# Kernel tuning notes

Hardware: AMD Instinct MI355X
Metric: run time of the kernel (lower is better)

The kernel has to match this reference:

```python
import jax, jax.numpy as jnp
import numpy as np

TOPK = 13
ALPHA = 1.0
BETA = 6.0
NUM_CLASSES = 80
EPS = 1e-9


def _make_boxes(key, shape, max_half):
    # shape = (..., 4): build valid x1y1x2y2 boxes inside a 640x640 image
    kc, ks = jax.random.split(key)
    centers = jax.random.uniform(kc, shape[:-1] + (2,), minval=30.0, maxval=610.0)
    halves = jax.random.uniform(ks, shape[:-1] + (2,), minval=2.0, maxval=max_half)
    return jnp.concatenate([centers - halves, centers + halves], axis=-1)


def setup_inputs() -> dict:
    key = jax.random.key(0)
    k1, k2, k3, k4, k5 = jax.random.split(key, 5)
    B, L, C, n = 16, 8400, NUM_CLASSES, 128
    pred_scores = jax.random.uniform(k1, (B, L, C), dtype=jnp.float32)
    pred_bboxes = _make_boxes(k2, (B, L, 4), 60.0)
    anchor_points = jax.random.uniform(k3, (L, 2), minval=0.0, maxval=640.0)
    gt_labels = jax.random.randint(k4, (B, n), 0, C, dtype=jnp.int32)
    gt_bboxes = _make_boxes(k5, (B, n, 4), 120.0)
    pad_gt_mask = jnp.ones((B, n, 1), dtype=jnp.float32)
    return {"pred_scores": pred_scores, "pred_bboxes": pred_bboxes,
            "anchor_points": anchor_points, "gt_labels": gt_labels,
            "gt_bboxes": gt_bboxes, "pad_gt_mask": pad_gt_mask}


def _batch_iou(box1, box2, eps=1e-9):
    # box1: [B, n, 4], box2: [B, L, 4] -> iou [B, n, L]
    b1 = box1[:, :, None]  # [B,n,1,4]
    b2 = box2[:, None]     # [B,1,L,4]
    x1y1 = jnp.maximum(b1[..., 0:2], b2[..., 0:2])
    x2y2 = jnp.minimum(b1[..., 2:4], b2[..., 2:4])
    overlap = jnp.prod(jnp.clip(x2y2 - x1y1, 0.0), axis=-1)
    area1 = jnp.prod(jnp.clip(b1[..., 2:4] - b1[..., 0:2], 0.0), axis=-1)
    area2 = jnp.prod(jnp.clip(b2[..., 2:4] - b2[..., 0:2], 0.0), axis=-1)
    return overlap / (area1 + area2 - overlap + eps)


def _points_in_bboxes(points, bboxes, eps=EPS):
    # points: [L,2], bboxes: [B,n,4] -> [B,n,L] float
    x = points[None, None, :, 0]
    y = points[None, None, :, 1]
    xmin = bboxes[..., 0:1]; ymin = bboxes[..., 1:2]
    xmax = bboxes[..., 2:3]; ymax = bboxes[..., 3:4]
    l = x - xmin; t = y - ymin; r = xmax - x; b = ymax - y
    d = jnp.minimum(jnp.minimum(l, t), jnp.minimum(r, b))
    return (d > eps).astype(bboxes.dtype)


def _gather_topk(metrics, topk, topk_mask):
    # metrics: [B,n,L] -> one-hot membership of per-gt topk anchors [B,n,L]
    L = metrics.shape[-1]
    _, topk_idxs = jax.lax.top_k(metrics, topk)          # [B,n,topk]
    is_in_topk = jax.nn.one_hot(topk_idxs, L, dtype=metrics.dtype).sum(-2)
    return is_in_topk * topk_mask


def reference(pred_scores, pred_bboxes, anchor_points, gt_labels, gt_bboxes, pad_gt_mask):
    B, n, _ = gt_bboxes.shape
    L = pred_bboxes.shape[1]
    # pairwise IoU between gts and predicted boxes: [B,n,L]
    ious = _batch_iou(gt_bboxes, pred_bboxes)
    # per-gt class scores gathered from pred_scores: [B,n,L]
    scores_cl = jnp.transpose(pred_scores, (0, 2, 1))                 # [B,C,L]
    bbox_cls_scores = jnp.take_along_axis(scores_cl, gt_labels[:, :, None].astype(jnp.int32), axis=1)
    # task-aligned metric
    alignment = (bbox_cls_scores ** ALPHA) * (ious ** BETA)
    is_in_gts = _points_in_bboxes(anchor_points, gt_bboxes)           # [B,n,L]
    is_in_topk = _gather_topk(alignment * is_in_gts, TOPK, pad_gt_mask)
    mask_positive = is_in_topk * is_in_gts * pad_gt_mask              # [B,n,L]
    # resolve anchors assigned to multiple gts: keep max-IoU gt
    mask_pos_sum = mask_positive.sum(-2)                              # [B,L]
    is_max_iou = jnp.transpose(jax.nn.one_hot(jnp.argmax(ious, axis=-2), n, dtype=ious.dtype), (0, 2, 1))
    mask_positive = jnp.where((mask_pos_sum[:, None, :] > 1), is_max_iou, mask_positive)
    mask_pos_sum = mask_positive.sum(-2)
    # assignment
    assigned_gt_index = jnp.argmax(mask_positive, axis=-2)            # [B,L]
    flat_idx = assigned_gt_index + jnp.arange(B, dtype=assigned_gt_index.dtype)[:, None] * n
    assigned_labels = jnp.reshape(gt_labels, (-1,))[flat_idx]
    assigned_labels = jnp.where(mask_pos_sum > 0, assigned_labels, NUM_CLASSES)
    assigned_bboxes = jnp.reshape(gt_bboxes, (-1, 4))[flat_idx]       # [B,L,4]
    assigned_scores = jax.nn.one_hot(assigned_labels, NUM_CLASSES + 1, dtype=pred_scores.dtype)[..., :NUM_CLASSES]
    # rescale scores by normalized alignment metric
    align_m = alignment * mask_positive
    max_metric = align_m.max(-1, keepdims=True)                       # [B,n,1]
    max_iou = (ious * mask_positive).max(-1, keepdims=True)           # [B,n,1]
    align_m = (align_m / (max_metric + EPS)) * max_iou
    assigned_scores = assigned_scores * align_m.max(-2)[..., None]    # [B,L,C]
    return assigned_labels, assigned_bboxes, assigned_scores
```

## Files before the change

### kernel.cpp

```cpp
#include <hip/hip_runtime.h>
#include <stdint.h>

#define BB    16
#define NGT   128
#define LL    8400
#define CC    80
#define KTOP  13
#define FEPS  1e-9f
#define NCELL 10
#define SLOTS 128

typedef float vfloat4 __attribute__((ext_vector_type(4)));

__device__ __forceinline__ float iou_f(float4 g, float4 p) {
    float ix0 = fmaxf(g.x, p.x);
    float iy0 = fmaxf(g.y, p.y);
    float ix1 = fminf(g.z, p.z);
    float iy1 = fminf(g.w, p.w);
    float ow = fmaxf(ix1 - ix0, 0.0f);
    float oh = fmaxf(iy1 - iy0, 0.0f);
    float ov = ow * oh;
    float a1 = fmaxf(g.z - g.x, 0.0f) * fmaxf(g.w - g.y, 0.0f);
    float a2 = fmaxf(p.z - p.x, 0.0f) * fmaxf(p.w - p.y, 0.0f);
    return ov / (a1 + a2 - ov + FEPS);
}

#define SORT2(a,b) { unsigned long long _t=(a), _u=(b); (a)=(_u>_t)?_u:_t; (b)=(_u>_t)?_t:_u; }
#define INSERT13(key) do { unsigned long long _k=(key); if (_k > k12) { k12=_k; \
    SORT2(k11,k12) SORT2(k10,k11) SORT2(k9,k10) SORT2(k8,k9) SORT2(k7,k8) \
    SORT2(k6,k7)  SORT2(k5,k6)  SORT2(k4,k5) SORT2(k3,k4) SORT2(k2,k3) \
    SORT2(k1,k2)  SORT2(k0,k1) } } while(0)
#define POP13() { k0=k1;k1=k2;k2=k3;k3=k4;k4=k5;k5=k6;k6=k7;k7=k8;k8=k9;k9=k10;k10=k11;k11=k12;k12=0ull; }

__global__ __launch_bounds__(256) void prep_kernel(
    const float2* __restrict__ anchors,
    int* __restrict__ bin_cnt,
    int* __restrict__ bins,
    int* __restrict__ zero_base,
    int  zero_words)
{
    int blk = blockIdx.x;
    int tid = threadIdx.x;
    if (blk < NCELL * NCELL) {
        __shared__ int lcnt;
        __shared__ int lbin[SLOTS];
        if (tid == 0) lcnt = 0;
        __syncthreads();
        int cy = blk / NCELL, cx = blk % NCELL;
        for (int j = tid; j < LL; j += 256) {
            float2 ap = anchors[j];
            int acx = min(max((int)(ap.x * (1.0f / 64.0f)), 0), NCELL - 1);
            int acy = min(max((int)(ap.y * (1.0f / 64.0f)), 0), NCELL - 1);
            if (acx == cx && acy == cy) {
                int s = atomicAdd(&lcnt, 1);
                if (s < SLOTS) lbin[s] = j;
            }
        }
        __syncthreads();
        if (tid == 0) bin_cnt[blk] = lcnt;
        int n = min(lcnt, SLOTS);
        for (int s = tid; s < n; s += 256) bins[blk * SLOTS + s] = lbin[s];
    } else {
        int t = (blk - NCELL * NCELL) * 256 + tid;
        if (t < zero_words) zero_base[t] = 0;
    }
}

__global__ __launch_bounds__(256) void select_kernel(
    const float*  __restrict__ pred_scores,
    const float4* __restrict__ pred_bboxes,
    const float2* __restrict__ anchors,
    const int*    __restrict__ gt_labels,
    const float4* __restrict__ gt_bboxes,
    const int*    __restrict__ bin_cnt,
    const int*    __restrict__ bins,
    int* __restrict__ claim_count,
    int* __restrict__ claimant)
{
    int tid  = threadIdx.x;
    int wave = tid >> 6;
    int lane = tid & 63;
    int row  = blockIdx.x;
    int b    = row >> 7;
    int i_gt = row & (NGT - 1);

    float4 g  = gt_bboxes[row];
    int label = gt_labels[row];
    const float*  sc = pred_scores + (size_t)b * LL * CC + label;
    const float4* pb = pred_bboxes + (size_t)b * LL;

    unsigned long long k0=0,k1=0,k2=0,k3=0,k4=0,k5=0,k6=0,k7=0,k8=0,k9=0,k10=0,k11=0,k12=0;

    int cx0 = min(max((int)(g.x * (1.0f / 64.0f)), 0), NCELL - 1);
    int cy0 = min(max((int)(g.y * (1.0f / 64.0f)), 0), NCELL - 1);
    int cx1 = min(max((int)(g.z * (1.0f / 64.0f)), 0), NCELL - 1);
    int cy1 = min(max((int)(g.w * (1.0f / 64.0f)), 0), NCELL - 1);
    int ncx = cx1 - cx0 + 1;
    int ncells = ncx * (cy1 - cy0 + 1);

    bool ovf = false;
    for (int c = 0; c < ncells; ++c) {
        int cell = (cy0 + c / ncx) * NCELL + (cx0 + c % ncx);
        if (bin_cnt[cell] > SLOTS) ovf = true;
    }

    if (ovf) {
        for (int j = tid; j < LL; j += 256) {
            float2 ap = anchors[j];
            float d = fminf(fminf(ap.x - g.x, ap.y - g.y),
                            fminf(g.z - ap.x, g.w - ap.y));
            if (d > FEPS) {
                float4 p = pb[j];
                float io = iou_f(g, p);
                if (io > 0.0f) {
                    float s  = sc[(size_t)j * CC];
                    float i2 = io * io;
                    float met = s * (i2 * i2 * i2);
                    if (met > 0.0f)
                        INSERT13(((unsigned long long)__float_as_uint(met) << 32)
                                 | (unsigned)(~(unsigned)j));
                }
            }
        }
    } else {
        for (int c = wave; c < ncells; c += 4) {
            int cell = (cy0 + c / ncx) * NCELL + (cx0 + c % ncx);
            int cnt  = bin_cnt[cell];
            const int* cb = bins + cell * SLOTS;
            for (int s = lane; s < cnt; s += 64) {
                int j = cb[s];
                float2 ap = anchors[j];
                float d = fminf(fminf(ap.x - g.x, ap.y - g.y),
                                fminf(g.z - ap.x, g.w - ap.y));
                if (d > FEPS) {
                    float4 p = pb[j];
                    float io = iou_f(g, p);
                    if (io > 0.0f) {
                        float sv = sc[(size_t)j * CC];
                        float i2 = io * io;
                        float met = sv * (i2 * i2 * i2);
                        if (met > 0.0f)
                            INSERT13(((unsigned long long)__float_as_uint(met) << 32)
                                     | (unsigned)(~(unsigned)j));
                    }
                }
            }
        }
    }

    __shared__ unsigned long long wkeys[4 * KTOP];
    for (int r = 0; r < KTOP; ++r) {
        unsigned long long head = k0;
        unsigned long long m = head;
#pragma unroll
        for (int off = 1; off < 64; off <<= 1) {
            unsigned long long o = __shfl_xor(m, off, 64);
            if (o > m) m = o;
        }
        if (head == m && m != 0ull) POP13();
        if (lane == 0) wkeys[wave * KTOP + r] = m;
    }
    __syncthreads();

    if (wave == 0) {
        unsigned long long kk = (lane < 4 * KTOP) ? wkeys[lane] : 0ull;
        unsigned long long winner = 0ull;
        for (int r = 0; r < KTOP; ++r) {
            unsigned long long m = kk;
#pragma unroll
            for (int off = 1; off < 64; off <<= 1) {
                unsigned long long o = __shfl_xor(m, off, 64);
                if (o > m) m = o;
            }
            if (kk == m && m != 0ull) kk = 0ull;
            if (lane == r) winner = m;
        }

        int jwv = -1;
        if (lane < KTOP && winner != 0ull)
            jwv = (int)(~(unsigned)(winner & 0xFFFFFFFFull));

        bool marked = false;
        for (int r = 0; r < KTOP; ++r) {
            int jv = __shfl(jwv, r, 64);
            if (jv == lane) marked = true;
        }
        unsigned long long nonpos = ~__ballot(marked);
        int P = __popcll(__ballot(jwv >= 0));

        int base = b * LL;
        if (jwv >= 0) {
            atomicAdd(claim_count + base + jwv, 1);
            atomicMax(claimant + base + jwv, i_gt);
        }
        if (lane >= P && lane < KTOP) {
            unsigned long long mask = nonpos;
            for (int t = 0; t < lane - P; ++t) mask &= mask - 1ull;
            int jf = __ffsll(mask) - 1;
            float2 ap = anchors[jf];
            float d = fminf(fminf(ap.x - g.x, ap.y - g.y),
                            fminf(g.z - ap.x, g.w - ap.y));
            if (d > FEPS) {
                atomicAdd(claim_count + base + jf, 1);
                atomicMax(claimant + base + jf, i_gt);
            }
        }
    }
}

__global__ __launch_bounds__(256) void resolve_kernel(
    const float*  __restrict__ pred_scores,
    const float4* __restrict__ pred_bboxes,
    const int*    __restrict__ gt_labels,
    const float4* __restrict__ gt_bboxes,
    const int*    __restrict__ claim_count,
    const int*    __restrict__ claimant,
    int*      __restrict__ assigned_gt,
    float*    __restrict__ align_anchor,
    unsigned* __restrict__ max_metric,
    unsigned* __restrict__ max_iou,
    float*    __restrict__ out_labels,
    float4*   __restrict__ out_bboxes)
{
    int b = blockIdx.y;
    int j = blockIdx.x * 256 + threadIdx.x;

    __shared__ float4 gbox[NGT];
    __shared__ int    glab[NGT];
    if (threadIdx.x < NGT) {
        gbox[threadIdx.x] = gt_bboxes[b * NGT + threadIdx.x];
        glab[threadIdx.x] = gt_labels[b * NGT + threadIdx.x];
    }
    __syncthreads();
    if (j >= LL) return;

    int idx = b * LL + j;
    int cnt = claim_count[idx];
    int g = -1;
    float4 p = pred_bboxes[(size_t)b * LL + j];

    if (cnt == 1) {
        g = claimant[idx];
    } else if (cnt > 1) {
        float best = -1.0f;
        int   bi   = 0;
        for (int i = 0; i < NGT; ++i) {
            float iou = iou_f(gbox[i], p);
            if (iou > best) { best = iou; bi = i; }
        }
        g = bi;
    }
    assigned_gt[idx] = g;

    int label; float4 bb;
    if (g >= 0) {
        float iou = iou_f(gbox[g], p);
        float s   = pred_scores[((size_t)b * LL + j) * CC + glab[g]];
        float i2  = iou * iou;
        float al  = s * (i2 * i2 * i2);
        align_anchor[idx] = al;
        atomicMax(max_metric + b * NGT + g, __float_as_uint(al));
        atomicMax(max_iou    + b * NGT + g, __float_as_uint(iou));
        label = glab[g];
        bb    = gbox[g];
    } else {
        label = CC;
        bb    = gbox[0];
    }
    out_labels[idx] = (float)label;
    out_bboxes[idx] = bb;
}

__global__ __launch_bounds__(256) void score_kernel(
    const int*    __restrict__ gt_labels,
    const int*    __restrict__ assigned_gt,
    const float*  __restrict__ align_anchor,
    const unsigned* __restrict__ max_metric,
    const unsigned* __restrict__ max_iou,
    float*  __restrict__ out_scores)
{
    __shared__ int   s_lab[64];
    __shared__ float s_f[64];

    if (threadIdx.x < 64) {
        int t = blockIdx.x * 64 + threadIdx.x;
        int b = t / LL;
        int g = assigned_gt[t];
        int label = CC;
        float f = 0.0f;
        if (g >= 0) {
            label = gt_labels[b * NGT + g];
            float mm = __uint_as_float(max_metric[b * NGT + g]);
            float mi = __uint_as_float(max_iou[b * NGT + g]);
            f = align_anchor[t] / (mm + FEPS) * mi;
        }
        s_lab[threadIdx.x] = label;
        s_f[threadIdx.x]   = f;
    }
    __syncthreads();

    vfloat4* outs = (vfloat4*)(out_scores + (size_t)blockIdx.x * 64 * CC);
#pragma unroll
    for (int k = 0; k < 5; ++k) {
        int i = k * 256 + threadIdx.x;
        int anchor = i / (CC / 4);
        int c4     = i % (CC / 4);
        int lab    = s_lab[anchor];
        vfloat4 v = {0.f, 0.f, 0.f, 0.f};
        int rel = lab - c4 * 4;
        if (rel >= 0 && rel < 4) v[rel] = s_f[anchor];
        outs[i] = v;
    }
}

extern "C" void kernel_launch(void* const* d_in, const int* in_sizes, int n_in,
                              void* d_out, int out_size, void* d_ws, size_t ws_size,
                              hipStream_t stream)
{
    const float*  pred_scores = (const float*)d_in[0];
    const float4* pred_bboxes = (const float4*)d_in[1];
    const float2* anchors     = (const float2*)d_in[2];
    const int*    gt_labels   = (const int*)d_in[3];
    const float4* gt_bboxes   = (const float4*)d_in[4];

    char* w = (char*)d_ws;
    int*      claim_count  = (int*)(w);
    int*      claimant     = (int*)(w + 537600);
    unsigned* max_metric   = (unsigned*)(w + 1075200);
    unsigned* max_iou      = (unsigned*)(w + 1083392);
    int*      assigned_gt  = (int*)(w + 1091584);
    float*    align_anchor = (float*)(w + 1629184);
    int*      bin_cnt      = (int*)(w + 2166784);
    int*      bins         = (int*)(w + 2167296);

    const int ZERO_WORDS = 1091584 / 4;

    float*  out        = (float*)d_out;
    float*  out_labels = out;
    float4* out_bboxes = (float4*)(out + (size_t)BB * LL);
    float*  out_scores = out + (size_t)BB * LL * 5;

    int zero_blocks = (ZERO_WORDS + 255) / 256;
    prep_kernel<<<NCELL * NCELL + zero_blocks, 256, 0, stream>>>(
        anchors, bin_cnt, bins, (int*)w, ZERO_WORDS);

    select_kernel<<<BB * NGT, 256, 0, stream>>>(
        pred_scores, pred_bboxes, anchors, gt_labels, gt_bboxes,
        bin_cnt, bins, claim_count, claimant);

    dim3 gridC((LL + 255) / 256, BB);
    resolve_kernel<<<gridC, 256, 0, stream>>>(
        pred_scores, pred_bboxes, gt_labels, gt_bboxes,
        claim_count, claimant, assigned_gt, align_anchor, max_metric, max_iou,
        out_labels, out_bboxes);

    score_kernel<<<(BB * LL) / 64, 256, 0, stream>>>(
        gt_labels, assigned_gt, align_anchor, max_metric, max_iou, out_scores);
}
```

Baseline: 96.03 us.

## Pack per-batch cell records with anchor and pred box for contiguous loads

The prep kernel now builds, for each batch and grid cell, a contiguous record array holding each anchor's coordinates, its index, and its predicted box, instead of a plain index list. The select kernel's binned path reads these packed records sequentially rather than doing indirect gathers of anchors and predicted boxes. This removes two dependent scattered loads per candidate, but prep now launches 16 times as many binning blocks, each scanning all anchors, and the workspace grows accordingly. Cell counts are written only by the batch-0 blocks, which is valid because anchors are shared across batches.

After: 104.0 us. 1.08x slower.

```diff
diff --git a/kernel.cpp b/kernel.cpp
--- a/kernel.cpp
+++ b/kernel.cpp
@@ -34,34 +34,41 @@
 
 __global__ __launch_bounds__(256) void prep_kernel(
     const float2* __restrict__ anchors,
-    int* __restrict__ bin_cnt,
-    int* __restrict__ bins,
+    const float4* __restrict__ pred_bboxes,
+    int*     __restrict__ bin_cnt,
+    vfloat4* __restrict__ cellrec,
     int* __restrict__ zero_base,
     int  zero_words)
 {
     int blk = blockIdx.x;
     int tid = threadIdx.x;
-    if (blk < NCELL * NCELL) {
+    if (blk < BB * NCELL * NCELL) {
+        int b = blk / (NCELL * NCELL);
+        int c = blk % (NCELL * NCELL);
         __shared__ int lcnt;
-        __shared__ int lbin[SLOTS];
         if (tid == 0) lcnt = 0;
         __syncthreads();
-        int cy = blk / NCELL, cx = blk % NCELL;
+        int cy = c / NCELL, cx = c % NCELL;
+        vfloat4* rec = cellrec + (size_t)(b * NCELL * NCELL + c) * SLOTS * 2;
         for (int j = tid; j < LL; j += 256) {
             float2 ap = anchors[j];
             int acx = min(max((int)(ap.x * (1.0f / 64.0f)), 0), NCELL - 1);
             int acy = min(max((int)(ap.y * (1.0f / 64.0f)), 0), NCELL - 1);
             if (acx == cx && acy == cy) {
                 int s = atomicAdd(&lcnt, 1);
-                if (s < SLOTS) lbin[s] = j;
+                if (s < SLOTS) {
+                    float4 p = pred_bboxes[(size_t)b * LL + j];
+                    vfloat4 r0 = {ap.x, ap.y, __int_as_float(j), 0.0f};
+                    vfloat4 r1 = {p.x, p.y, p.z, p.w};
+                    rec[2 * s]     = r0;
+                    rec[2 * s + 1] = r1;
+                }
             }
         }
         __syncthreads();
-        if (tid == 0) bin_cnt[blk] = lcnt;
-        int n = min(lcnt, SLOTS);
-        for (int s = tid; s < n; s += 256) bins[blk * SLOTS + s] = lbin[s];
+        if (tid == 0 && b == 0) bin_cnt[c] = lcnt;
     } else {
-        int t = (blk - NCELL * NCELL) * 256 + tid;
+        int t = (blk - BB * NCELL * NCELL) * 256 + tid;
         if (t < zero_words) zero_base[t] = 0;
     }
 }
@@ -73,7 +80,7 @@
     const int*    __restrict__ gt_labels,
     const float4* __restrict__ gt_bboxes,
     const int*    __restrict__ bin_cnt,
-    const int*    __restrict__ bins,
+    const vfloat4* __restrict__ cellrec,
     int* __restrict__ claim_count,
     int* __restrict__ claimant)
 {
@@ -126,16 +133,17 @@
         for (int c = wave; c < ncells; c += 4) {
             int cell = (cy0 + c / ncx) * NCELL + (cx0 + c % ncx);
             int cnt  = bin_cnt[cell];
-            const int* cb = bins + cell * SLOTS;
+            const vfloat4* rec = cellrec + (size_t)(b * NCELL * NCELL + cell) * SLOTS * 2;
             for (int s = lane; s < cnt; s += 64) {
-                int j = cb[s];
-                float2 ap = anchors[j];
-                float d = fminf(fminf(ap.x - g.x, ap.y - g.y),
-                                fminf(g.z - ap.x, g.w - ap.y));
+                vfloat4 r0 = rec[2 * s];
+                float d = fminf(fminf(r0.x - g.x, r0.y - g.y),
+                                fminf(g.z - r0.x, g.w - r0.y));
                 if (d > FEPS) {
-                    float4 p = pb[j];
+                    vfloat4 r1 = rec[2 * s + 1];
+                    float4 p = {r1.x, r1.y, r1.z, r1.w};
                     float io = iou_f(g, p);
                     if (io > 0.0f) {
+                        int j = __float_as_int(r0.z);
                         float sv = sc[(size_t)j * CC];
                         float i2 = io * io;
                         float met = sv * (i2 * i2 * i2);
@@ -331,7 +339,7 @@
     int*      assigned_gt  = (int*)(w + 1091584);
     float*    align_anchor = (float*)(w + 1629184);
     int*      bin_cnt      = (int*)(w + 2166784);
-    int*      bins         = (int*)(w + 2167296);
+    vfloat4*  cellrec      = (vfloat4*)(w + 2167296);
 
     const int ZERO_WORDS = 1091584 / 4;
 
@@ -341,12 +349,12 @@
     float*  out_scores = out + (size_t)BB * LL * 5;
 
     int zero_blocks = (ZERO_WORDS + 255) / 256;
-    prep_kernel<<<NCELL * NCELL + zero_blocks, 256, 0, stream>>>(
-        anchors, bin_cnt, bins, (int*)w, ZERO_WORDS);
+    prep_kernel<<<BB * NCELL * NCELL + zero_blocks, 256, 0, stream>>>(
+        anchors, pred_bboxes, bin_cnt, cellrec, (int*)w, ZERO_WORDS);
 
     select_kernel<<<BB * NGT, 256, 0, stream>>>(
         pred_scores, pred_bboxes, anchors, gt_labels, gt_bboxes,
-        bin_cnt, bins, claim_count, claimant);
+        bin_cnt, cellrec, claim_count, claimant);
 
     dim3 gridC((LL + 255) / 256, BB);
     resolve_kernel<<<gridC, 256, 0, stream>>>(
```

## Flatten per-gt cell candidates into prefix-summed work list across block

Applied to the files above, without the earlier changes.

Before, each wave walked whole grid cells, so work was uneven across waves and lanes. Now one wave builds a shared list of the overlapping cells and a prefix sum of their bin counts, and all 256 threads stride over the flattened candidate list. Block indices are also remapped so consecutive blocks come from different batches, and the pred-box load is hoisted ahead of the inside-box test. The cost is an extra __syncthreads, a small linear search per candidate, and speculative loads of boxes for anchors that later fail the test.

New measurement: 99.77 us. 1.04x slower.

```diff
diff --git a/kernel.cpp b/kernel.cpp
--- a/kernel.cpp
+++ b/kernel.cpp
@@ -80,7 +80,8 @@
     int tid  = threadIdx.x;
     int wave = tid >> 6;
     int lane = tid & 63;
-    int row  = blockIdx.x;
+    int blk  = blockIdx.x;
+    int row  = (blk & 15) * NGT + (blk >> 4);
     int b    = row >> 7;
     int i_gt = row & (NGT - 1);
 
@@ -98,13 +99,30 @@
     int ncx = cx1 - cx0 + 1;
     int ncells = ncx * (cy1 - cy0 + 1);
 
-    bool ovf = false;
-    for (int c = 0; c < ncells; ++c) {
-        int cell = (cy0 + c / ncx) * NCELL + (cx0 + c % ncx);
-        if (bin_cnt[cell] > SLOTS) ovf = true;
-    }
-
-    if (ovf) {
+    __shared__ int s_cells[32];
+    __shared__ int s_pfx[33];
+    __shared__ int s_ovf;
+    if (tid < 64) {
+        int cnt = 0;
+        if (lane == 0) s_ovf = 0;
+        if (lane < ncells) {
+            int cell = (cy0 + lane / ncx) * NCELL + (cx0 + lane % ncx);
+            s_cells[lane] = cell;
+            int c = bin_cnt[cell];
+            if (c > SLOTS) s_ovf = 1;
+            cnt = min(c, SLOTS);
+        }
+        int x = cnt;
+        for (int off = 1; off < 32; off <<= 1) {
+            int y = __shfl_up(x, off, 64);
+            if (lane >= off) x += y;
+        }
+        if (lane < ncells) s_pfx[lane + 1] = x;
+        if (lane == 0) s_pfx[0] = 0;
+    }
+    __syncthreads();
+
+    if (s_ovf) {
         for (int j = tid; j < LL; j += 256) {
             float2 ap = anchors[j];
             float d = fminf(fminf(ap.x - g.x, ap.y - g.y),
@@ -123,27 +141,23 @@
             }
         }
     } else {
-        for (int c = wave; c < ncells; c += 4) {
-            int cell = (cy0 + c / ncx) * NCELL + (cx0 + c % ncx);
-            int cnt  = bin_cnt[cell];
-            const int* cb = bins + cell * SLOTS;
-            for (int s = lane; s < cnt; s += 64) {
-                int j = cb[s];
-                float2 ap = anchors[j];
-                float d = fminf(fminf(ap.x - g.x, ap.y - g.y),
-                                fminf(g.z - ap.x, g.w - ap.y));
-                if (d > FEPS) {
-                    float4 p = pb[j];
-                    float io = iou_f(g, p);
-                    if (io > 0.0f) {
-                        float sv = sc[(size_t)j * CC];
-                        float i2 = io * io;
-                        float met = sv * (i2 * i2 * i2);
-                        if (met > 0.0f)
-                            INSERT13(((unsigned long long)__float_as_uint(met) << 32)
-                                     | (unsigned)(~(unsigned)j));
-                    }
-                }
+        int total = s_pfx[ncells];
+        for (int t = tid; t < total; t += 256) {
+            int c = 0;
+            while (t >= s_pfx[c + 1]) ++c;
+            int j = bins[s_cells[c] * SLOTS + (t - s_pfx[c])];
+            float2 ap = anchors[j];
+            float4 p  = pb[j];
+            float d  = fminf(fminf(ap.x - g.x, ap.y - g.y),
+                             fminf(g.z - ap.x, g.w - ap.y));
+            float io = iou_f(g, p);
+            if (d > FEPS && io > 0.0f) {
+                float sv = sc[(size_t)j * CC];
+                float i2 = io * io;
+                float met = sv * (i2 * i2 * i2);
+                if (met > 0.0f)
+                    INSERT13(((unsigned long long)__float_as_uint(met) << 32)
+                             | (unsigned)(~(unsigned)j));
             }
         }
     }
```

## Compact candidates into shared list, store anchor coords in bins, swizzle block order

Applied to the files above, without the earlier changes.

The select kernel no longer keeps a 13-deep register sorted list in every thread of all four waves. Each thread now appends candidate keys to a shared-memory list through an atomic counter, and a single wave builds the top-13 from that list, with a full-scan fallback on overflow. The prep kernel also stores anchor coordinates next to the bin indices so the point-in-box test reads them contiguously, and block indices are swizzled to interleave batches. This is meant to cut register pressure and the cost of sorted insertion per thread, but it adds shared-memory atomics and serialises the top-k merge onto one wave.

Result: faster. 86.02 us (-10.4%).

```diff
diff --git a/kernel.cpp b/kernel.cpp
--- a/kernel.cpp
+++ b/kernel.cpp
@@ -9,6 +9,7 @@
 #define FEPS  1e-9f
 #define NCELL 10
 #define SLOTS 128
+#define LCAP  2048
 
 typedef float vfloat4 __attribute__((ext_vector_type(4)));
 
@@ -34,8 +35,9 @@
 
 __global__ __launch_bounds__(256) void prep_kernel(
     const float2* __restrict__ anchors,
-    int* __restrict__ bin_cnt,
-    int* __restrict__ bins,
+    int*    __restrict__ bin_cnt,
+    int*    __restrict__ bins_j,
+    float2* __restrict__ bins_xy,
     int* __restrict__ zero_base,
     int  zero_words)
 {
@@ -59,7 +61,11 @@
         __syncthreads();
         if (tid == 0) bin_cnt[blk] = lcnt;
         int n = min(lcnt, SLOTS);
-        for (int s = tid; s < n; s += 256) bins[blk * SLOTS + s] = lbin[s];
+        for (int s = tid; s < n; s += 256) {
+            int j = lbin[s];
+            bins_j[blk * SLOTS + s]  = j;
+            bins_xy[blk * SLOTS + s] = anchors[j];
+        }
     } else {
         int t = (blk - NCELL * NCELL) * 256 + tid;
         if (t < zero_words) zero_base[t] = 0;
@@ -73,14 +79,16 @@
     const int*    __restrict__ gt_labels,
     const float4* __restrict__ gt_bboxes,
     const int*    __restrict__ bin_cnt,
-    const int*    __restrict__ bins,
+    const int*    __restrict__ bins_j,
+    const float2* __restrict__ bins_xy,
     int* __restrict__ claim_count,
     int* __restrict__ claimant)
 {
     int tid  = threadIdx.x;
     int wave = tid >> 6;
     int lane = tid & 63;
-    int row  = blockIdx.x;
+    int blk  = blockIdx.x;
+    int row  = (blk & 15) * NGT + (blk >> 4);
     int b    = row >> 7;
     int i_gt = row & (NGT - 1);
 
@@ -89,7 +97,10 @@
     const float*  sc = pred_scores + (size_t)b * LL * CC + label;
     const float4* pb = pred_bboxes + (size_t)b * LL;
 
-    unsigned long long k0=0,k1=0,k2=0,k3=0,k4=0,k5=0,k6=0,k7=0,k8=0,k9=0,k10=0,k11=0,k12=0;
+    __shared__ unsigned long long s_list[LCAP];
+    __shared__ int s_cnt;
+    if (tid == 0) s_cnt = 0;
+    __syncthreads();
 
     int cx0 = min(max((int)(g.x * (1.0f / 64.0f)), 0), NCELL - 1);
     int cy0 = min(max((int)(g.y * (1.0f / 64.0f)), 0), NCELL - 1);
@@ -104,31 +115,43 @@
         if (bin_cnt[cell] > SLOTS) ovf = true;
     }
 
-    if (ovf) {
-        for (int j = tid; j < LL; j += 256) {
-            float2 ap = anchors[j];
-            float d = fminf(fminf(ap.x - g.x, ap.y - g.y),
-                            fminf(g.z - ap.x, g.w - ap.y));
-            if (d > FEPS) {
-                float4 p = pb[j];
-                float io = iou_f(g, p);
-                if (io > 0.0f) {
-                    float s  = sc[(size_t)j * CC];
-                    float i2 = io * io;
-                    float met = s * (i2 * i2 * i2);
-                    if (met > 0.0f)
-                        INSERT13(((unsigned long long)__float_as_uint(met) << 32)
-                                 | (unsigned)(~(unsigned)j));
-                }
-            }
-        }
-    } else {
+    if (!ovf) {
         for (int c = wave; c < ncells; c += 4) {
             int cell = (cy0 + c / ncx) * NCELL + (cx0 + c % ncx);
             int cnt  = bin_cnt[cell];
-            const int* cb = bins + cell * SLOTS;
+            const float2* bxy = bins_xy + cell * SLOTS;
+            const int*    bj  = bins_j  + cell * SLOTS;
             for (int s = lane; s < cnt; s += 64) {
-                int j = cb[s];
+                float2 ap = bxy[s];
+                float d = fminf(fminf(ap.x - g.x, ap.y - g.y),
+                                fminf(g.z - ap.x, g.w - ap.y));
+                if (d > FEPS) {
+                    int j = bj[s];
+                    float4 p = pb[j];
+                    float io = iou_f(g, p);
+                    if (io > 0.0f) {
+                        float sv = sc[(size_t)j * CC];
+                        float i2 = io * io;
+                        float met = sv * (i2 * i2 * i2);
+                        if (met > 0.0f) {
+                            int slot = atomicAdd(&s_cnt, 1);
+                            if (slot < LCAP)
+                                s_list[slot] =
+                                    ((unsigned long long)__float_as_uint(met) << 32)
+                                    | (unsigned)(~(unsigned)j);
+                        }
+                    }
+                }
+            }
+        }
+    }
+    __syncthreads();
+
+    if (wave == 0) {
+        unsigned long long k0=0,k1=0,k2=0,k3=0,k4=0,k5=0,k6=0,k7=0,k8=0,k9=0,k10=0,k11=0,k12=0;
+        int n = s_cnt;
+        if (ovf || n > LCAP) {
+            for (int j = lane; j < LL; j += 64) {
                 float2 ap = anchors[j];
                 float d = fminf(fminf(ap.x - g.x, ap.y - g.y),
                                 fminf(g.z - ap.x, g.w - ap.y));
@@ -136,43 +159,30 @@
                     float4 p = pb[j];
                     float io = iou_f(g, p);
                     if (io > 0.0f) {
-                        float sv = sc[(size_t)j * CC];
+                        float s  = sc[(size_t)j * CC];
                         float i2 = io * io;
-                        float met = sv * (i2 * i2 * i2);
+                        float met = s * (i2 * i2 * i2);
                         if (met > 0.0f)
                             INSERT13(((unsigned long long)__float_as_uint(met) << 32)
                                      | (unsigned)(~(unsigned)j));
                     }
                 }
             }
-        }
-    }
-
-    __shared__ unsigned long long wkeys[4 * KTOP];
-    for (int r = 0; r < KTOP; ++r) {
-        unsigned long long head = k0;
-        unsigned long long m = head;
-#pragma unroll
-        for (int off = 1; off < 64; off <<= 1) {
-            unsigned long long o = __shfl_xor(m, off, 64);
-            if (o > m) m = o;
-        }
-        if (head == m && m != 0ull) POP13();
-        if (lane == 0) wkeys[wave * KTOP + r] = m;
-    }
-    __syncthreads();
-
-    if (wave == 0) {
-        unsigned long long kk = (lane < 4 * KTOP) ? wkeys[lane] : 0ull;
+        } else {
+            for (int t = lane; t < n; t += 64)
+                INSERT13(s_list[t]);
+        }
+
         unsigned long long winner = 0ull;
         for (int r = 0; r < KTOP; ++r) {
-            unsigned long long m = kk;
+            unsigned long long head = k0;
+            unsigned long long m = head;
 #pragma unroll
             for (int off = 1; off < 64; off <<= 1) {
                 unsigned long long o = __shfl_xor(m, off, 64);
                 if (o > m) m = o;
             }
-            if (kk == m && m != 0ull) kk = 0ull;
+            if (head == m && m != 0ull) POP13();
             if (lane == r) winner = m;
         }
 
@@ -331,7 +341,8 @@
     int*      assigned_gt  = (int*)(w + 1091584);
     float*    align_anchor = (float*)(w + 1629184);
     int*      bin_cnt      = (int*)(w + 2166784);
-    int*      bins         = (int*)(w + 2167296);
+    int*      bins_j       = (int*)(w + 2167296);
+    float2*   bins_xy      = (float2*)(w + 2218496);
 
     const int ZERO_WORDS = 1091584 / 4;
 
@@ -342,11 +353,11 @@
 
     int zero_blocks = (ZERO_WORDS + 255) / 256;
     prep_kernel<<<NCELL * NCELL + zero_blocks, 256, 0, stream>>>(
-        anchors, bin_cnt, bins, (int*)w, ZERO_WORDS);
+        anchors, bin_cnt, bins_j, bins_xy, (int*)w, ZERO_WORDS);
 
     select_kernel<<<BB * NGT, 256, 0, stream>>>(
         pred_scores, pred_bboxes, anchors, gt_labels, gt_bboxes,
-        bin_cnt, bins, claim_count, claimant);
+        bin_cnt, bins_j, bins_xy, claim_count, claimant);
 
     dim3 gridC((LL + 255) / 256, BB);
     resolve_kernel<<<gridC, 256, 0, stream>>>(
```
